# Optimization experiments

Measured on AMD Instinct MI355X. Metric: run time of the kernel, lower is better.

## Reference

```python
import jax, jax.numpy as jnp
import numpy as np

B, H, W, DM = 4, 64, 64, 96
DS, DC, K = 16, 3, 4
DI = DM            # expand = 1.0
DTR = 6            # ceil(96/16)


def setup_inputs() -> dict:
    key = jax.random.key(0)
    ks = jax.random.split(key, 12)
    s = 0.02
    # dt bias init exactly as MS2D.dt_init: dt ~ exp(U*(log(max)-log(min))+log(min)); inv softplus
    dt = jnp.exp(jax.random.uniform(ks[5], (K, DI)) * (np.log(0.1) - np.log(0.001)) + np.log(0.001))
    dt = jnp.clip(dt, 1e-4, None)
    inv_dt = dt + jnp.log(-jnp.expm1(-dt))
    A_logs = jnp.log(jnp.broadcast_to(jnp.arange(1, DS + 1, dtype=jnp.float32), (K, DI, DS)))
    return {
        "x": jax.random.normal(ks[0], (B, H, W, DM), jnp.float32),
        "in_proj_w": jax.random.normal(ks[1], (2 * DI, DM), jnp.float32) * s,
        "conv_w": jax.random.normal(ks[2], (DI, 1, DC, DC), jnp.float32) * s,
        "conv_b": jnp.zeros((DI,), jnp.float32),
        "x_proj_weight": jax.random.normal(ks[3], (K, DTR + 2 * DS, DI), jnp.float32) * s,
        "dt_projs_weight": jax.random.uniform(ks[4], (K, DI, DTR), minval=-1.0, maxval=1.0) * (DTR ** -0.5),
        "dt_projs_bias": inv_dt,
        "A_logs": A_logs,
        "Ds": jnp.ones((K, DI), jnp.float32),
        "out_norm_w": jnp.ones((DI,), jnp.float32),
        "out_norm_b": jnp.zeros((DI,), jnp.float32),
        "out_proj_w": jax.random.normal(ks[6], (DM, DI), jnp.float32) * s,
    }


def _ms2d(x, in_proj_w, conv_w, conv_b, x_proj_weight, dt_projs_weight,
          dt_projs_bias, A_logs, Ds, out_norm_w, out_norm_b, out_proj_w):
    Bb, Hh, Ww, _ = x.shape
    L = Hh * Ww
    # in_proj -> (x, z) gating split
    xz = x @ in_proj_w.T                      # (B,H,W,2*DI)
    xc, z = jnp.split(xz, 2, axis=-1)
    xc = jnp.transpose(xc, (0, 3, 1, 2))      # (B,DI,H,W)
    xc = jax.lax.conv_general_dilated(
        xc, conv_w, (1, 1), 'SAME', feature_group_count=xc.shape[1],
        dimension_numbers=('NCHW', 'OIHW', 'NCHW')) + conv_b[None, :, None, None]
    xc = jax.nn.silu(xc)
    d = xc.shape[1]
    # 4-directional scan sequences: hw, wh, and their reverses
    x_hw = xc.reshape(Bb, d, L)
    x_wh = jnp.transpose(xc, (0, 1, 3, 2)).reshape(Bb, d, L)
    x2 = jnp.stack([x_hw, x_wh], axis=1)          # (B,2,d,L)
    xs = jnp.concatenate([x2, jnp.flip(x2, axis=-1)], axis=1)  # (B,4,d,L)
    x_dbl = jnp.einsum('bkdl,kcd->bkcl', xs, x_proj_weight)
    dtr = dt_projs_weight.shape[2]
    n = A_logs.shape[2]
    dts, Bs, Cs = jnp.split(x_dbl, [dtr, dtr + n], axis=2)     # (B,4,r,L),(B,4,N,L),(B,4,N,L)
    dts = jnp.einsum('bkrl,kdr->bkdl', dts, dt_projs_weight)
    delta = jax.nn.softplus(dts + dt_projs_bias[None, :, :, None])  # (B,4,d,L)
    A = -jnp.exp(A_logs)                                        # (4,d,N)
    # time-major for scan
    u_t = jnp.moveaxis(xs, -1, 0)       # (L,B,4,d)
    dl_t = jnp.moveaxis(delta, -1, 0)
    B_t = jnp.moveaxis(Bs, -1, 0)       # (L,B,4,N)
    C_t = jnp.moveaxis(Cs, -1, 0)

    def step(h, inp):                   # h: (B,4,d,N)
        u, dl, b, c = inp
        dA = jnp.exp(dl[..., None] * A)
        h = h * dA + (dl * u)[..., None] * b[:, :, None, :]
        y = jnp.einsum('bkdn,bkn->bkd', h, c)
        return h, y

    h0 = jnp.zeros((Bb, 4, d, n), xs.dtype)
    _, ys = jax.lax.scan(step, h0, (u_t, dl_t, B_t, C_t))
    ys = jnp.moveaxis(ys, 0, -1)        # (B,4,d,L)
    ys = ys + Ds[None, :, :, None] * xs  # skip D*u
    inv_y = jnp.flip(ys[:, 2:4], axis=-1)

    def wh2hw(t):  # undo the (W,H) raster order
        return jnp.transpose(t.reshape(Bb, d, Ww, Hh), (0, 1, 3, 2)).reshape(Bb, d, L)

    y = ys[:, 0] + inv_y[:, 0] + wh2hw(ys[:, 1]) + wh2hw(inv_y[:, 1])
    y = jnp.transpose(y, (0, 2, 1)).reshape(Bb, Hh, Ww, d)
    mu = y.mean(-1, keepdims=True)
    var = y.var(-1, keepdims=True)
    y = (y - mu) / jnp.sqrt(var + 1e-5) * out_norm_w + out_norm_b
    y = y * jax.nn.silu(z)
    return y @ out_proj_w.T


def reference(x, in_proj_w, conv_w, conv_b, x_proj_weight, dt_projs_weight,
              dt_projs_bias, A_logs, Ds, out_norm_w, out_norm_b, out_proj_w):
    return _ms2d(x, in_proj_w, conv_w, conv_b, x_proj_weight, dt_projs_weight,
                 dt_projs_bias, A_logs, Ds, out_norm_w, out_norm_b, out_proj_w)
```

## Files before the change

### kernel.cpp

```cpp
#include <hip/hip_runtime.h>
#include <math.h>


#define LQ 4096
#define NCH 128
#define LCH 32

__device__ __forceinline__ float sigmoid_f(float x){ return 1.0f/(1.0f + __expf(-x)); }
__device__ __forceinline__ float silu_f(float x){ return x * sigmoid_f(x); }
__device__ __forceinline__ float softplus_f(float x){ return (x > 20.0f) ? x : __logf(1.0f + __expf(x)); }

__device__ __forceinline__ int pos_of(int k, int i){
  switch(k & 3){
    case 0: return i;
    case 1: return ((i & 63) << 6) | (i >> 6);
    case 2: return LQ - 1 - i;
    default: { int j = LQ - 1 - i; return ((j & 63) << 6) | (j >> 6); }
  }
}

__global__ __launch_bounds__(256) void k_inproj(const float* __restrict__ x,
                                                const float* __restrict__ wproj,
                                                float* __restrict__ xc,
                                                float* __restrict__ zb){
  __shared__ float a_s[64*97];
  __shared__ float w_s[192*97];
  const int t = threadIdx.x;
  const int row0 = blockIdx.x * 64;
  for (int e = t*4; e < 64*96; e += 1024){
    float4 v = *(const float4*)(x + row0*96 + e);
    int r = e/96, c = e%96;
    float* p = a_s + r*97 + c;
    p[0]=v.x; p[1]=v.y; p[2]=v.z; p[3]=v.w;
  }
  for (int e = t*4; e < 192*96; e += 1024){
    float4 v = *(const float4*)(wproj + e);
    int r = e/96, c = e%96;
    float* p = w_s + r*97 + c;
    p[0]=v.x; p[1]=v.y; p[2]=v.z; p[3]=v.w;
  }
  __syncthreads();
  const int tr = t >> 5, tc = t & 31;
  float acc[8][6];
  #pragma unroll
  for (int i=0;i<8;i++){
    #pragma unroll
    for (int j=0;j<6;j++) acc[i][j]=0.f;
  }
  for (int kk=0; kk<96; kk++){
    float a[8], b[6];
    #pragma unroll
    for (int i=0;i<8;i++) a[i] = a_s[(tr*8+i)*97+kk];
    #pragma unroll
    for (int j=0;j<6;j++) b[j] = w_s[(tc*6+j)*97+kk];
    #pragma unroll
    for (int i=0;i<8;i++){
      #pragma unroll
      for (int j=0;j<6;j++) acc[i][j] += a[i]*b[j];
    }
  }
  #pragma unroll
  for (int i=0;i<8;i++){
    int row = row0 + tr*8 + i;
    #pragma unroll
    for (int j=0;j<6;j++){
      int c = tc*6+j;
      float v = acc[i][j];
      if (c < 96) xc[row*96+c] = v;
      else        zb[row*96+(c-96)] = v;
    }
  }
}

__global__ __launch_bounds__(256) void k_conv(const float* __restrict__ xc,
                                              const float* __restrict__ cw,
                                              const float* __restrict__ cb,
                                              float* __restrict__ u){
  int e = blockIdx.x*256 + threadIdx.x;
  int d0 = (e % 24) * 4;
  int p = e / 24;
  int w = p & 63, h = (p >> 6) & 63, b = p >> 12;
  float cwv[4][9];
  #pragma unroll
  for (int q=0;q<4;q++){
    #pragma unroll
    for (int tp=0;tp<9;tp++) cwv[q][tp] = cw[(d0+q)*9+tp];
  }
  float4 acc = make_float4(cb[d0], cb[d0+1], cb[d0+2], cb[d0+3]);
  #pragma unroll
  for (int kh=0; kh<3; kh++){
    int hh = h + kh - 1;
    if (hh < 0 || hh > 63) continue;
    #pragma unroll
    for (int kw=0; kw<3; kw++){
      int ww = w + kw - 1;
      if (ww < 0 || ww > 63) continue;
      float4 v = *(const float4*)(xc + ((size_t)((b<<12) + (hh<<6) + ww))*96 + d0);
      int tp = kh*3+kw;
      acc.x += v.x*cwv[0][tp]; acc.y += v.y*cwv[1][tp];
      acc.z += v.z*cwv[2][tp]; acc.w += v.w*cwv[3][tp];
    }
  }
  float4 o = make_float4(silu_f(acc.x), silu_f(acc.y), silu_f(acc.z), silu_f(acc.w));
  *(float4*)(u + (size_t)p*96 + d0) = o;
}

__global__ __launch_bounds__(128) void k_proj(const float* __restrict__ u,
                                              const float* __restrict__ xpw,
                                              float* __restrict__ dts,
                                              float* __restrict__ Bsb,
                                              float* __restrict__ Csb){
  __shared__ float u_s[64*97];
  __shared__ float w_s[40*97];
  const int t = threadIdx.x;
  const int blk = blockIdx.x;
  const int pt = blk & 63, k = (blk >> 6) & 3, b = blk >> 8;
  const int p0 = pt * 64;
  for (int e = t*4; e < 64*96; e += 512){
    int pp = e/96, c = e%96;
    float4 v = *(const float4*)(u + ((size_t)((b<<12) + p0 + pp))*96 + c);
    float* p = u_s + pp*97 + c;
    p[0]=v.x; p[1]=v.y; p[2]=v.z; p[3]=v.w;
  }
  for (int e = t*4; e < 40*96; e += 512){
    int r = e/96, c = e%96;
    float4 v = (r < 38) ? *(const float4*)(xpw + (k*38+r)*96 + c)
                        : make_float4(0,0,0,0);
    float* p = w_s + r*97 + c;
    p[0]=v.x; p[1]=v.y; p[2]=v.z; p[3]=v.w;
  }
  __syncthreads();
  const int posg = t & 15, cg = t >> 4;
  float acc[4][5];
  #pragma unroll
  for (int i=0;i<4;i++){
    #pragma unroll
    for (int j=0;j<5;j++) acc[i][j]=0.f;
  }
  for (int dd=0; dd<96; dd++){
    float uu[4], wv[5];
    #pragma unroll
    for (int i=0;i<4;i++) uu[i] = u_s[(posg*4+i)*97+dd];
    #pragma unroll
    for (int j=0;j<5;j++) wv[j] = w_s[(cg*5+j)*97+dd];
    #pragma unroll
    for (int i=0;i<4;i++){
      #pragma unroll
      for (int j=0;j<5;j++) acc[i][j] += uu[i]*wv[j];
    }
  }
  #pragma unroll
  for (int i=0;i<4;i++){
    int p = p0 + posg*4 + i;
    int base = ((b*4+k)<<12) + p;
    #pragma unroll
    for (int j=0;j<5;j++){
      int c = cg*5 + j;
      float v = acc[i][j];
      if (c < 6)       dts[(size_t)base*6 + c] = v;
      else if (c < 22) Bsb[(size_t)base*16 + (c-6)] = v;
      else if (c < 38) Csb[(size_t)base*16 + (c-22)] = v;
    }
  }
}

__device__ __forceinline__ void pow8(float r, int nh, float* e){
  e[0]=r;
  e[1]=r*r;
  e[2]=e[1]*r;
  e[3]=e[1]*e[1];
  e[4]=e[3]*r;
  e[5]=e[3]*e[1];
  e[6]=e[3]*e[2];
  e[7]=e[3]*e[3];
  float m = nh ? e[7] : 1.0f;
  #pragma unroll
  for (int j=0;j<8;j++) e[j] *= m;
}

template<bool FAST>
__device__ __forceinline__ void scanA_loop(const float* up, const float2* dtp,
    const float4* Bp, long ustep, long dtstep, long bstep,
    const float* dtw, float bias, int nh, const float* An, float* h, float& sdelta){
  #pragma unroll 4
  for (int il=0; il<LCH; il++){
    const float uv = *up;
    float2 q0 = dtp[0], q1 = dtp[1], q2 = dtp[2];
    float accd = bias + dtw[0]*q0.x + dtw[1]*q0.y + dtw[2]*q1.x
                      + dtw[3]*q1.y + dtw[4]*q2.x + dtw[5]*q2.y;
    float delta = softplus_f(accd);
    sdelta += delta;
    float du = delta * uv;
    float4 b0 = Bp[0], b1 = Bp[1];
    float Bv[8] = {b0.x,b0.y,b0.z,b0.w, b1.x,b1.y,b1.z,b1.w};
    float e[8];
    if (FAST){ pow8(__expf(-delta), nh, e); }
    else {
      #pragma unroll
      for (int n=0;n<8;n++) e[n] = __expf(delta*An[n]);
    }
    #pragma unroll
    for (int n=0;n<8;n++) h[n] = h[n]*e[n] + du*Bv[n];
    up += ustep; dtp += dtstep; Bp += bstep;
  }
}

__global__ __launch_bounds__(384) void k_scanA(const float* __restrict__ u,
                                               const float* __restrict__ dts,
                                               const float* __restrict__ Bsb,
                                               const float* __restrict__ dtw_g,
                                               const float* __restrict__ dtb_g,
                                               const float* __restrict__ Alogs,
                                               float* __restrict__ S,
                                               float* __restrict__ sumd){
  const int t = threadIdx.x;
  const int c2 = t / 192;
  const int lane = t & 63;
  const int wv3 = (t % 192) >> 6;
  const int nh = (lane >> 5) & 1;
  const int d = wv3*32 + (lane & 31);
  const int blk = blockIdx.x;
  const int bk = blk >> 6;
  const int k = bk & 3, b = bk >> 2;
  const int chunk = ((blk & 63) << 1) | c2;
  float An[8];
  bool fast = true;
  #pragma unroll
  for (int j=0;j<8;j++){
    int n = nh*8 + j;
    An[j] = -__expf(Alogs[(k*96+d)*16+n]);
    fast = fast && (fabsf(An[j] + (float)(n+1)) < 1e-3f*(float)(n+1));
  }
  int wfast = __all(fast ? 1 : 0);
  float dtw[6];
  #pragma unroll
  for (int r=0;r<6;r++) dtw[r] = dtw_g[(k*96+d)*6+r];
  const float bias = dtb_g[k*96+d];
  const int i0 = chunk*LCH;
  const int pb = pos_of(k, i0);
  const int pstep = pos_of(k, i0+1) - pb;
  const float* up = u + ((size_t)((b<<12)+pb))*96 + d;
  const float2* dtp = (const float2*)(dts + ((size_t)((bk<<12)+pb))*6);
  const float4* Bp = (const float4*)(Bsb + ((size_t)((bk<<12)+pb))*16) + nh*2;
  const long ustep = (long)pstep*96;
  const long dtstep = (long)pstep*3;
  const long bstep = (long)pstep*4;
  float h[8];
  #pragma unroll
  for (int n=0;n<8;n++) h[n]=0.f;
  float sdelta = 0.f;
  if (wfast) scanA_loop<true >(up,dtp,Bp,ustep,dtstep,bstep,dtw,bias,nh,An,h,sdelta);
  else       scanA_loop<false>(up,dtp,Bp,ustep,dtstep,bstep,dtw,bias,nh,An,h,sdelta);
  const int sb = (bk*NCH + chunk)*96 + d;
  float4* Sp = (float4*)(S + (size_t)sb*16 + nh*8);
  Sp[0] = make_float4(h[0],h[1],h[2],h[3]);
  Sp[1] = make_float4(h[4],h[5],h[6],h[7]);
  if (nh == 0) sumd[sb] = sdelta;
}

__global__ __launch_bounds__(256) void k_scanB(const float* __restrict__ S,
                                               const float* __restrict__ sumd,
                                               const float* __restrict__ Alogs,
                                               float* __restrict__ hinit){
  const int t = blockIdx.x*256 + threadIdx.x;
  const int n = t & 15;
  const int d = (t >> 4) % 96;
  const int bk = t / 1536;
  const int k = bk & 3;
  const float An = -__expf(Alogs[(k*96+d)*16+n]);
  float h = 0.f;
  for (int c=0;c<NCH;c++){
    const int sb = (bk*NCH + c)*96 + d;
    hinit[(size_t)sb*16+n] = h;
    float P = __expf(An * sumd[sb]);
    h = h*P + S[(size_t)sb*16+n];
  }
}

template<bool FAST>
__device__ __forceinline__ void scanC_loop(const float* up, const float2* dtp,
    const float4* Bp, const float4* Cp, float* yp,
    long ustep, long dtstep, long bstep,
    const float* dtw, float bias, int nh, const float* An, float* h){
  #pragma unroll 4
  for (int il=0; il<LCH; il++){
    const float uv = *up;
    float2 q0 = dtp[0], q1 = dtp[1], q2 = dtp[2];
    float accd = bias + dtw[0]*q0.x + dtw[1]*q0.y + dtw[2]*q1.x
                      + dtw[3]*q1.y + dtw[4]*q2.x + dtw[5]*q2.y;
    float delta = softplus_f(accd);
    float du = delta * uv;
    float4 b0 = Bp[0], b1 = Bp[1];
    float4 c0 = Cp[0], c1 = Cp[1];
    float Bv[8] = {b0.x,b0.y,b0.z,b0.w, b1.x,b1.y,b1.z,b1.w};
    float Cv[8] = {c0.x,c0.y,c0.z,c0.w, c1.x,c1.y,c1.z,c1.w};
    float e[8];
    if (FAST){ pow8(__expf(-delta), nh, e); }
    else {
      #pragma unroll
      for (int n=0;n<8;n++) e[n] = __expf(delta*An[n]);
    }
    float y8 = 0.f;
    #pragma unroll
    for (int n=0;n<8;n++){
      h[n] = h[n]*e[n] + du*Bv[n];
      y8 += h[n]*Cv[n];
    }
    float y = y8 + __shfl_xor(y8, 32, 64);
    if (nh == 0) *yp = y;
    up += ustep; dtp += dtstep; Bp += bstep; Cp += bstep; yp += ustep;
  }
}

__global__ __launch_bounds__(384) void k_scanC(const float* __restrict__ u,
                                               const float* __restrict__ dts,
                                               const float* __restrict__ Bsb,
                                               const float* __restrict__ Csb,
                                               const float* __restrict__ dtw_g,
                                               const float* __restrict__ dtb_g,
                                               const float* __restrict__ Alogs,
                                               const float* __restrict__ hinit,
                                               float* __restrict__ ys){
  const int t = threadIdx.x;
  const int c2 = t / 192;
  const int lane = t & 63;
  const int wv3 = (t % 192) >> 6;
  const int nh = (lane >> 5) & 1;
  const int d = wv3*32 + (lane & 31);
  const int blk = blockIdx.x;
  const int bk = blk >> 6;
  const int k = bk & 3, b = bk >> 2;
  const int chunk = ((blk & 63) << 1) | c2;
  float An[8];
  bool fast = true;
  #pragma unroll
  for (int j=0;j<8;j++){
    int n = nh*8 + j;
    An[j] = -__expf(Alogs[(k*96+d)*16+n]);
    fast = fast && (fabsf(An[j] + (float)(n+1)) < 1e-3f*(float)(n+1));
  }
  int wfast = __all(fast ? 1 : 0);
  float dtw[6];
  #pragma unroll
  for (int r=0;r<6;r++) dtw[r] = dtw_g[(k*96+d)*6+r];
  const float bias = dtb_g[k*96+d];
  const int i0 = chunk*LCH;
  const int pb = pos_of(k, i0);
  const int pstep = pos_of(k, i0+1) - pb;
  const float* up = u + ((size_t)((b<<12)+pb))*96 + d;
  const float2* dtp = (const float2*)(dts + ((size_t)((bk<<12)+pb))*6);
  const float4* Bp = (const float4*)(Bsb + ((size_t)((bk<<12)+pb))*16) + nh*2;
  const float4* Cp = (const float4*)(Csb + ((size_t)((bk<<12)+pb))*16) + nh*2;
  float* yp = ys + ((size_t)((bk<<12)+pb))*96 + d;
  const long ustep = (long)pstep*96;
  const long dtstep = (long)pstep*3;
  const long bstep = (long)pstep*4;
  float h[8];
  const int sb = (bk*NCH + chunk)*96 + d;
  const float4* Hp = (const float4*)(hinit + (size_t)sb*16 + nh*8);
  {
    float4 h0=Hp[0], h1=Hp[1];
    h[0]=h0.x;h[1]=h0.y;h[2]=h0.z;h[3]=h0.w;
    h[4]=h1.x;h[5]=h1.y;h[6]=h1.z;h[7]=h1.w;
  }
  if (wfast) scanC_loop<true >(up,dtp,Bp,Cp,yp,ustep,dtstep,bstep,dtw,bias,nh,An,h);
  else       scanC_loop<false>(up,dtp,Bp,Cp,yp,ustep,dtstep,bstep,dtw,bias,nh,An,h);
}

__global__ __launch_bounds__(256) void k_out(const float* __restrict__ ys,
                                             const float* __restrict__ ubuf,
                                             const float* __restrict__ Dsg,
                                             const float* __restrict__ zbuf,
                                             const float* __restrict__ nw,
                                             const float* __restrict__ nb,
                                             const float* __restrict__ wout,
                                             float* __restrict__ out){
  __shared__ float w_s[96*97];
  __shared__ float g_s[64*97];
  __shared__ float redA[256];
  __shared__ float redB[256];
  const int t = threadIdx.x;
  const int b = blockIdx.x >> 6;
  const int pt = blockIdx.x & 63;
  const int p0 = pt * 64;
  for (int e=t*4; e<96*96; e+=1024){
    float4 v = *(const float4*)(wout+e);
    int r=e/96, c=e%96;
    float* p = w_s + r*97 + c;
    p[0]=v.x; p[1]=v.y; p[2]=v.z; p[3]=v.w;
  }
  const int pos2 = t >> 2, lane4 = t & 3, d0 = lane4*24;
  const int p = p0 + pos2;
  float yv[24];
  float s1=0.f, s2=0.f;
  #pragma unroll
  for (int i=0;i<24;i+=4){
    float4 a = make_float4(0,0,0,0);
    #pragma unroll
    for (int kk=0;kk<4;kk++){
      float4 v = *(const float4*)(ys + ((size_t)(((b*4+kk)<<12) + p))*96 + d0 + i);
      a.x+=v.x; a.y+=v.y; a.z+=v.z; a.w+=v.w;
    }
    float4 uv = *(const float4*)(ubuf + ((size_t)((b<<12)+p))*96 + d0 + i);
    #pragma unroll
    for (int q=0;q<4;q++){
      int dd = d0+i+q;
      float sD = Dsg[dd] + Dsg[96+dd] + Dsg[192+dd] + Dsg[288+dd];
      float uq = (q==0)?uv.x:(q==1)?uv.y:(q==2)?uv.z:uv.w;
      float* aq = (q==0)?&a.x:(q==1)?&a.y:(q==2)?&a.z:&a.w;
      *aq += sD * uq;
    }
    yv[i]=a.x; yv[i+1]=a.y; yv[i+2]=a.z; yv[i+3]=a.w;
    s1 += a.x+a.y+a.z+a.w;
    s2 += a.x*a.x + a.y*a.y + a.z*a.z + a.w*a.w;
  }
  redA[t]=s1; redB[t]=s2;
  __syncthreads();
  if (lane4 < 2){ redA[t]+=redA[t+2]; redB[t]+=redB[t+2]; }
  __syncthreads();
  if (lane4 < 1){ redA[t]+=redA[t+1]; redB[t]+=redB[t+1]; }
  __syncthreads();
  const float mu = redA[pos2*4] * (1.0f/96.0f);
  const float var = redB[pos2*4] * (1.0f/96.0f) - mu*mu;
  const float rstd = rsqrtf(var + 1e-5f);
  #pragma unroll
  for (int i=0;i<24;i+=4){
    float4 zv = *(const float4*)(zbuf + ((size_t)((b<<12)+p))*96 + d0 + i);
    float zz[4] = {zv.x,zv.y,zv.z,zv.w};
    #pragma unroll
    for (int q=0;q<4;q++){
      int d = d0+i+q;
      float yn = (yv[i+q]-mu)*rstd*nw[d] + nb[d];
      g_s[pos2*97 + d] = yn * silu_f(zz[q]);
    }
  }
  __syncthreads();
  const int posg = t >> 5, mg = t & 31;
  float acc[8][3];
  #pragma unroll
  for (int i=0;i<8;i++){
    #pragma unroll
    for (int j=0;j<3;j++) acc[i][j]=0.f;
  }
  for (int dd=0; dd<96; dd++){
    float g8[8], w3[3];
    #pragma unroll
    for (int i=0;i<8;i++) g8[i] = g_s[(posg*8+i)*97+dd];
    #pragma unroll
    for (int j=0;j<3;j++) w3[j] = w_s[(mg*3+j)*97+dd];
    #pragma unroll
    for (int i=0;i<8;i++){
      #pragma unroll
      for (int j=0;j<3;j++) acc[i][j] += g8[i]*w3[j];
    }
  }
  #pragma unroll
  for (int i=0;i<8;i++){
    int prow = p0 + posg*8 + i;
    #pragma unroll
    for (int j=0;j<3;j++){
      out[((size_t)((b<<12)+prow))*96 + mg*3 + j] = acc[i][j];
    }
  }
}

extern "C" void kernel_launch(void* const* d_in, const int* in_sizes, int n_in,
                              void* d_out, int out_size, void* d_ws, size_t ws_size,
                              hipStream_t stream) {
  (void)in_sizes; (void)n_in; (void)out_size; (void)ws_size;
  const float* x   = (const float*)d_in[0];
  const float* ipw = (const float*)d_in[1];
  const float* cw  = (const float*)d_in[2];
  const float* cb  = (const float*)d_in[3];
  const float* xpw = (const float*)d_in[4];
  const float* dtw = (const float*)d_in[5];
  const float* dtb = (const float*)d_in[6];
  const float* alg = (const float*)d_in[7];
  const float* dsg = (const float*)d_in[8];
  const float* nw  = (const float*)d_in[9];
  const float* nb  = (const float*)d_in[10];
  const float* wo  = (const float*)d_in[11];
  float* out = (float*)d_out;

  float* w = (float*)d_ws;
  size_t off = 0;
  float* z_b    = w + off; off += 1572864;
  float* u_b    = w + off; off += 1572864;
  float* dts_b  = w + off; off += 393216;
  float* Bs_b   = w + off; off += 1048576;
  float* Cs_b   = w + off; off += 1048576;
  float* hin_b  = w + off; off += 3145728;
  float* ys_b   = w + off; off += 6291456;
  float* xc_b   = ys_b;
  float* S_b    = ys_b + 1572864;
  float* sumd_b = ys_b + 1572864 + 3145728;

  k_inproj<<<256, 256, 0, stream>>>(x, ipw, xc_b, z_b);
  k_conv  <<<1536, 256, 0, stream>>>(xc_b, cw, cb, u_b);
  k_proj  <<<1024, 128, 0, stream>>>(u_b, xpw, dts_b, Bs_b, Cs_b);
  k_scanA <<<1024, 384, 0, stream>>>(u_b, dts_b, Bs_b, dtw, dtb, alg, S_b, sumd_b);
  k_scanB <<<96, 256, 0, stream>>>(S_b, sumd_b, alg, hin_b);
  k_scanC <<<1024, 384, 0, stream>>>(u_b, dts_b, Bs_b, Cs_b, dtw, dtb, alg, hin_b, ys_b);
  k_out   <<<256, 256, 0, stream>>>(ys_b, u_b, dsg, z_b, nw, nb, wo, out);
}
```

Measured before the change: 273.9 us.

## Stage scan inputs in LDS, precompute delta terms cooperatively, split GEMM blocks

Both scan kernels now load a 64-step tile of u, dt-projection and B/C rows into shared memory, using coalesced float4 loads along the scan order. All 384 threads then compute softplus(delta), delta*u and exp(-delta) for the tile before the recurrence runs. This removes the strided per-thread global loads and the duplicate delta computation that the two n-halves each did. The in-projection and output kernels are split into twice as many smaller blocks for more parallelism, and the output kernel's LayerNorm reduction switches from shared memory to wavefront shuffles. The cost is larger LDS use per scan block, which may lower occupancy, plus an extra barrier.

```diff
diff --git a/kernel.cpp b/kernel.cpp
--- a/kernel.cpp
+++ b/kernel.cpp
@@ -19,56 +19,67 @@
   }
 }
 
+__device__ __forceinline__ void pow8(float r, int nh, float* e){
+  e[0]=r;
+  e[1]=r*r;
+  e[2]=e[1]*r;
+  e[3]=e[1]*e[1];
+  e[4]=e[3]*r;
+  e[5]=e[3]*e[1];
+  e[6]=e[3]*e[2];
+  e[7]=e[3]*e[3];
+  float m = nh ? e[7] : 1.0f;
+  #pragma unroll
+  for (int j=0;j<8;j++) e[j] *= m;
+}
+
 __global__ __launch_bounds__(256) void k_inproj(const float* __restrict__ x,
                                                 const float* __restrict__ wproj,
                                                 float* __restrict__ xc,
                                                 float* __restrict__ zb){
   __shared__ float a_s[64*97];
-  __shared__ float w_s[192*97];
+  __shared__ float w_s[96*97];
   const int t = threadIdx.x;
-  const int row0 = blockIdx.x * 64;
+  const int row0 = (blockIdx.x >> 1) * 64;
+  const int ch = blockIdx.x & 1;
   for (int e = t*4; e < 64*96; e += 1024){
-    float4 v = *(const float4*)(x + row0*96 + e);
+    float4 v = *(const float4*)(x + (size_t)row0*96 + e);
     int r = e/96, c = e%96;
     float* p = a_s + r*97 + c;
     p[0]=v.x; p[1]=v.y; p[2]=v.z; p[3]=v.w;
   }
-  for (int e = t*4; e < 192*96; e += 1024){
-    float4 v = *(const float4*)(wproj + e);
+  for (int e = t*4; e < 96*96; e += 1024){
+    float4 v = *(const float4*)(wproj + (size_t)ch*96*96 + e);
     int r = e/96, c = e%96;
     float* p = w_s + r*97 + c;
     p[0]=v.x; p[1]=v.y; p[2]=v.z; p[3]=v.w;
   }
   __syncthreads();
   const int tr = t >> 5, tc = t & 31;
-  float acc[8][6];
+  float acc[8][3];
   #pragma unroll
   for (int i=0;i<8;i++){
     #pragma unroll
-    for (int j=0;j<6;j++) acc[i][j]=0.f;
+    for (int j=0;j<3;j++) acc[i][j]=0.f;
   }
   for (int kk=0; kk<96; kk++){
-    float a[8], b[6];
+    float a[8], b[3];
     #pragma unroll
     for (int i=0;i<8;i++) a[i] = a_s[(tr*8+i)*97+kk];
     #pragma unroll
-    for (int j=0;j<6;j++) b[j] = w_s[(tc*6+j)*97+kk];
+    for (int j=0;j<3;j++) b[j] = w_s[(tc*3+j)*97+kk];
     #pragma unroll
     for (int i=0;i<8;i++){
       #pragma unroll
-      for (int j=0;j<6;j++) acc[i][j] += a[i]*b[j];
-    }
-  }
+      for (int j=0;j<3;j++) acc[i][j] += a[i]*b[j];
+    }
+  }
+  float* dst = ch ? zb : xc;
   #pragma unroll
   for (int i=0;i<8;i++){
     int row = row0 + tr*8 + i;
     #pragma unroll
-    for (int j=0;j<6;j++){
-      int c = tc*6+j;
-      float v = acc[i][j];
-      if (c < 96) xc[row*96+c] = v;
-      else        zb[row*96+(c-96)] = v;
-    }
+    for (int j=0;j<3;j++) dst[(size_t)row*96 + tc*3 + j] = acc[i][j];
   }
 }
 
@@ -164,47 +175,6 @@
   }
 }
 
-__device__ __forceinline__ void pow8(float r, int nh, float* e){
-  e[0]=r;
-  e[1]=r*r;
-  e[2]=e[1]*r;
-  e[3]=e[1]*e[1];
-  e[4]=e[3]*r;
-  e[5]=e[3]*e[1];
-  e[6]=e[3]*e[2];
-  e[7]=e[3]*e[3];
-  float m = nh ? e[7] : 1.0f;
-  #pragma unroll
-  for (int j=0;j<8;j++) e[j] *= m;
-}
-
-template<bool FAST>
-__device__ __forceinline__ void scanA_loop(const float* up, const float2* dtp,
-    const float4* Bp, long ustep, long dtstep, long bstep,
-    const float* dtw, float bias, int nh, const float* An, float* h, float& sdelta){
-  #pragma unroll 4
-  for (int il=0; il<LCH; il++){
-    const float uv = *up;
-    float2 q0 = dtp[0], q1 = dtp[1], q2 = dtp[2];
-    float accd = bias + dtw[0]*q0.x + dtw[1]*q0.y + dtw[2]*q1.x
-                      + dtw[3]*q1.y + dtw[4]*q2.x + dtw[5]*q2.y;
-    float delta = softplus_f(accd);
-    sdelta += delta;
-    float du = delta * uv;
-    float4 b0 = Bp[0], b1 = Bp[1];
-    float Bv[8] = {b0.x,b0.y,b0.z,b0.w, b1.x,b1.y,b1.z,b1.w};
-    float e[8];
-    if (FAST){ pow8(__expf(-delta), nh, e); }
-    else {
-      #pragma unroll
-      for (int n=0;n<8;n++) e[n] = __expf(delta*An[n]);
-    }
-    #pragma unroll
-    for (int n=0;n<8;n++) h[n] = h[n]*e[n] + du*Bv[n];
-    up += ustep; dtp += dtstep; Bp += bstep;
-  }
-}
-
 __global__ __launch_bounds__(384) void k_scanA(const float* __restrict__ u,
                                                const float* __restrict__ dts,
                                                const float* __restrict__ Bsb,
@@ -213,16 +183,63 @@
                                                const float* __restrict__ Alogs,
                                                float* __restrict__ S,
                                                float* __restrict__ sumd){
+  __shared__ float du_s[64*96];
+  __shared__ float r_s[64*96];
+  __shared__ float dt_s[64*8];
+  __shared__ float B_s[64*16];
+  __shared__ float sd_part[4*96];
   const int t = threadIdx.x;
+  const int blk = blockIdx.x;
+  const int bk = blk >> 6;
+  const int k = bk & 3, b = bk >> 2;
+  const int chunk0 = (blk & 63) << 1;
+  for (int e = t*4; e < 64*96; e += 1536){
+    int row = e/96, c = e%96;
+    int p = pos_of(k, (chunk0 + (row>>5))*LCH + (row&31));
+    float4 v = *(const float4*)(u + ((size_t)((b<<12)+p))*96 + c);
+    float* dst = du_s + row*96 + c;
+    dst[0]=v.x; dst[1]=v.y; dst[2]=v.z; dst[3]=v.w;
+  }
+  {
+    int row = t/6, j = t - row*6;
+    int p = pos_of(k, (chunk0 + (row>>5))*LCH + (row&31));
+    dt_s[row*8+j] = dts[((size_t)((bk<<12)+p))*6 + j];
+  }
+  if (t < 256){
+    int row = t>>2, q = t&3;
+    int p = pos_of(k, (chunk0 + (row>>5))*LCH + (row&31));
+    float4 v = *(const float4*)(Bsb + ((size_t)((bk<<12)+p))*16 + q*4);
+    *(float4*)(B_s + row*16 + q*4) = v;
+  }
+  __syncthreads();
+  {
+    const int d = t % 96, g = t / 96;
+    const int c2 = g >> 1, il0 = (g & 1) * 16;
+    float dtwv[6];
+    #pragma unroll
+    for (int r=0;r<6;r++) dtwv[r] = dtw_g[(k*96+d)*6+r];
+    const float bias = dtb_g[k*96+d];
+    float sd = 0.f;
+    #pragma unroll 4
+    for (int il = il0; il < il0+16; il++){
+      int row = c2*32 + il;
+      const float* dr = dt_s + row*8;
+      float accd = bias + dr[0]*dtwv[0] + dr[1]*dtwv[1] + dr[2]*dtwv[2]
+                        + dr[3]*dtwv[3] + dr[4]*dtwv[4] + dr[5]*dtwv[5];
+      float delta = softplus_f(accd);
+      sd += delta;
+      int idx = row*96 + d;
+      du_s[idx] = delta * du_s[idx];
+      r_s[idx] = __expf(-delta);
+    }
+    sd_part[g*96 + d] = sd;
+  }
+  __syncthreads();
   const int c2 = t / 192;
   const int lane = t & 63;
   const int wv3 = (t % 192) >> 6;
   const int nh = (lane >> 5) & 1;
   const int d = wv3*32 + (lane & 31);
-  const int blk = blockIdx.x;
-  const int bk = blk >> 6;
-  const int k = bk & 3, b = bk >> 2;
-  const int chunk = ((blk & 63) << 1) | c2;
   float An[8];
   bool fast = true;
   #pragma unroll
@@ -232,30 +249,46 @@
     fast = fast && (fabsf(An[j] + (float)(n+1)) < 1e-3f*(float)(n+1));
   }
   int wfast = __all(fast ? 1 : 0);
-  float dtw[6];
-  #pragma unroll
-  for (int r=0;r<6;r++) dtw[r] = dtw_g[(k*96+d)*6+r];
-  const float bias = dtb_g[k*96+d];
-  const int i0 = chunk*LCH;
-  const int pb = pos_of(k, i0);
-  const int pstep = pos_of(k, i0+1) - pb;
-  const float* up = u + ((size_t)((b<<12)+pb))*96 + d;
-  const float2* dtp = (const float2*)(dts + ((size_t)((bk<<12)+pb))*6);
-  const float4* Bp = (const float4*)(Bsb + ((size_t)((bk<<12)+pb))*16) + nh*2;
-  const long ustep = (long)pstep*96;
-  const long dtstep = (long)pstep*3;
-  const long bstep = (long)pstep*4;
   float h[8];
   #pragma unroll
   for (int n=0;n<8;n++) h[n]=0.f;
-  float sdelta = 0.f;
-  if (wfast) scanA_loop<true >(up,dtp,Bp,ustep,dtstep,bstep,dtw,bias,nh,An,h,sdelta);
-  else       scanA_loop<false>(up,dtp,Bp,ustep,dtstep,bstep,dtw,bias,nh,An,h,sdelta);
-  const int sb = (bk*NCH + chunk)*96 + d;
+  const float* dup = du_s + c2*32*96 + d;
+  const float* rp  = r_s  + c2*32*96 + d;
+  const float* Bb  = B_s + c2*32*16 + nh*8;
+  if (wfast){
+    #pragma unroll 4
+    for (int il=0; il<LCH; il++){
+      float r = rp[il*96];
+      float du = dup[il*96];
+      const float4* Bp = (const float4*)(Bb + il*16);
+      float4 b0 = Bp[0], b1 = Bp[1];
+      float Bv[8] = {b0.x,b0.y,b0.z,b0.w, b1.x,b1.y,b1.z,b1.w};
+      float e[8];
+      pow8(r, nh, e);
+      #pragma unroll
+      for (int n=0;n<8;n++) h[n] = h[n]*e[n] + du*Bv[n];
+    }
+  } else {
+    #pragma unroll 2
+    for (int il=0; il<LCH; il++){
+      float r = rp[il*96];
+      float delta = -__logf(r);
+      float du = dup[il*96];
+      const float4* Bp = (const float4*)(Bb + il*16);
+      float4 b0 = Bp[0], b1 = Bp[1];
+      float Bv[8] = {b0.x,b0.y,b0.z,b0.w, b1.x,b1.y,b1.z,b1.w};
+      float e[8];
+      #pragma unroll
+      for (int n=0;n<8;n++) e[n] = __expf(delta*An[n]);
+      #pragma unroll
+      for (int n=0;n<8;n++) h[n] = h[n]*e[n] + du*Bv[n];
+    }
+  }
+  const int sb = (bk*NCH + chunk0 + c2)*96 + d;
   float4* Sp = (float4*)(S + (size_t)sb*16 + nh*8);
   Sp[0] = make_float4(h[0],h[1],h[2],h[3]);
   Sp[1] = make_float4(h[4],h[5],h[6],h[7]);
-  if (nh == 0) sumd[sb] = sdelta;
+  if (nh == 0) sumd[sb] = sd_part[(c2*2)*96 + d] + sd_part[(c2*2+1)*96 + d];
 }
 
 __global__ __launch_bounds__(256) void k_scanB(const float* __restrict__ S,
@@ -277,41 +310,6 @@
   }
 }
 
-template<bool FAST>
-__device__ __forceinline__ void scanC_loop(const float* up, const float2* dtp,
-    const float4* Bp, const float4* Cp, float* yp,
-    long ustep, long dtstep, long bstep,
-    const float* dtw, float bias, int nh, const float* An, float* h){
-  #pragma unroll 4
-  for (int il=0; il<LCH; il++){
-    const float uv = *up;
-    float2 q0 = dtp[0], q1 = dtp[1], q2 = dtp[2];
-    float accd = bias + dtw[0]*q0.x + dtw[1]*q0.y + dtw[2]*q1.x
-                      + dtw[3]*q1.y + dtw[4]*q2.x + dtw[5]*q2.y;
-    float delta = softplus_f(accd);
-    float du = delta * uv;
-    float4 b0 = Bp[0], b1 = Bp[1];
-    float4 c0 = Cp[0], c1 = Cp[1];
-    float Bv[8] = {b0.x,b0.y,b0.z,b0.w, b1.x,b1.y,b1.z,b1.w};
-    float Cv[8] = {c0.x,c0.y,c0.z,c0.w, c1.x,c1.y,c1.z,c1.w};
-    float e[8];
-    if (FAST){ pow8(__expf(-delta), nh, e); }
-    else {
-      #pragma unroll
-      for (int n=0;n<8;n++) e[n] = __expf(delta*An[n]);
-    }
-    float y8 = 0.f;
-    #pragma unroll
-    for (int n=0;n<8;n++){
-      h[n] = h[n]*e[n] + du*Bv[n];
-      y8 += h[n]*Cv[n];
-    }
-    float y = y8 + __shfl_xor(y8, 32, 64);
-    if (nh == 0) *yp = y;
-    up += ustep; dtp += dtstep; Bp += bstep; Cp += bstep; yp += ustep;
-  }
-}
-
 __global__ __launch_bounds__(384) void k_scanC(const float* __restrict__ u,
                                                const float* __restrict__ dts,
                                                const float* __restrict__ Bsb,
@@ -321,16 +319,62 @@
                                                const float* __restrict__ Alogs,
                                                const float* __restrict__ hinit,
                                                float* __restrict__ ys){
+  __shared__ float du_s[64*96];
+  __shared__ float r_s[64*96];
+  __shared__ float dt_s[64*8];
+  __shared__ float B_s[64*16];
+  __shared__ float C_s[64*16];
   const int t = threadIdx.x;
+  const int blk = blockIdx.x;
+  const int bk = blk >> 6;
+  const int k = bk & 3, b = bk >> 2;
+  const int chunk0 = (blk & 63) << 1;
+  for (int e = t*4; e < 64*96; e += 1536){
+    int row = e/96, c = e%96;
+    int p = pos_of(k, (chunk0 + (row>>5))*LCH + (row&31));
+    float4 v = *(const float4*)(u + ((size_t)((b<<12)+p))*96 + c);
+    float* dst = du_s + row*96 + c;
+    dst[0]=v.x; dst[1]=v.y; dst[2]=v.z; dst[3]=v.w;
+  }
+  {
+    int row = t/6, j = t - row*6;
+    int p = pos_of(k, (chunk0 + (row>>5))*LCH + (row&31));
+    dt_s[row*8+j] = dts[((size_t)((bk<<12)+p))*6 + j];
+  }
+  if (t < 256){
+    int row = t>>2, q = t&3;
+    int p = pos_of(k, (chunk0 + (row>>5))*LCH + (row&31));
+    float4 v = *(const float4*)(Bsb + ((size_t)((bk<<12)+p))*16 + q*4);
+    *(float4*)(B_s + row*16 + q*4) = v;
+    float4 w = *(const float4*)(Csb + ((size_t)((bk<<12)+p))*16 + q*4);
+    *(float4*)(C_s + row*16 + q*4) = w;
+  }
+  __syncthreads();
+  {
+    const int d = t % 96, g = t / 96;
+    const int c2 = g >> 1, il0 = (g & 1) * 16;
+    float dtwv[6];
+    #pragma unroll
+    for (int r=0;r<6;r++) dtwv[r] = dtw_g[(k*96+d)*6+r];
+    const float bias = dtb_g[k*96+d];
+    #pragma unroll 4
+    for (int il = il0; il < il0+16; il++){
+      int row = c2*32 + il;
+      const float* dr = dt_s + row*8;
+      float accd = bias + dr[0]*dtwv[0] + dr[1]*dtwv[1] + dr[2]*dtwv[2]
+                        + dr[3]*dtwv[3] + dr[4]*dtwv[4] + dr[5]*dtwv[5];
+      float delta = softplus_f(accd);
+      int idx = row*96 + d;
+      du_s[idx] = delta * du_s[idx];
+      r_s[idx] = __expf(-delta);
+    }
+  }
+  __syncthreads();
   const int c2 = t / 192;
   const int lane = t & 63;
   const int wv3 = (t % 192) >> 6;
   const int nh = (lane >> 5) & 1;
   const int d = wv3*32 + (lane & 31);
-  const int blk = blockIdx.x;
-  const int bk = blk >> 6;
-  const int k = bk & 3, b = bk >> 2;
-  const int chunk = ((blk & 63) << 1) | c2;
   float An[8];
   bool fast = true;
   #pragma unroll
@@ -340,21 +384,12 @@
     fast = fast && (fabsf(An[j] + (float)(n+1)) < 1e-3f*(float)(n+1));
   }
   int wfast = __all(fast ? 1 : 0);
-  float dtw[6];
-  #pragma unroll
-  for (int r=0;r<6;r++) dtw[r] = dtw_g[(k*96+d)*6+r];
-  const float bias = dtb_g[k*96+d];
+  const int chunk = chunk0 + c2;
   const int i0 = chunk*LCH;
   const int pb = pos_of(k, i0);
   const int pstep = pos_of(k, i0+1) - pb;
-  const float* up = u + ((size_t)((b<<12)+pb))*96 + d;
-  const float2* dtp = (const float2*)(dts + ((size_t)((bk<<12)+pb))*6);
-  const float4* Bp = (const float4*)(Bsb + ((size_t)((bk<<12)+pb))*16) + nh*2;
-  const float4* Cp = (const float4*)(Csb + ((size_t)((bk<<12)+pb))*16) + nh*2;
   float* yp = ys + ((size_t)((bk<<12)+pb))*96 + d;
-  const long ustep = (long)pstep*96;
-  const long dtstep = (long)pstep*3;
-  const long bstep = (long)pstep*4;
+  const long ystep = (long)pstep*96;
   float h[8];
   const int sb = (bk*NCH + chunk)*96 + d;
   const float4* Hp = (const float4*)(hinit + (size_t)sb*16 + nh*8);
@@ -363,8 +398,57 @@
     h[0]=h0.x;h[1]=h0.y;h[2]=h0.z;h[3]=h0.w;
     h[4]=h1.x;h[5]=h1.y;h[6]=h1.z;h[7]=h1.w;
   }
-  if (wfast) scanC_loop<true >(up,dtp,Bp,Cp,yp,ustep,dtstep,bstep,dtw,bias,nh,An,h);
-  else       scanC_loop<false>(up,dtp,Bp,Cp,yp,ustep,dtstep,bstep,dtw,bias,nh,An,h);
+  const float* dup = du_s + c2*32*96 + d;
+  const float* rp  = r_s  + c2*32*96 + d;
+  const float* Bb  = B_s + c2*32*16 + nh*8;
+  const float* Cb  = C_s + c2*32*16 + nh*8;
+  if (wfast){
+    #pragma unroll 4
+    for (int il=0; il<LCH; il++){
+      float r = rp[il*96];
+      float du = dup[il*96];
+      const float4* Bp = (const float4*)(Bb + il*16);
+      const float4* Cp = (const float4*)(Cb + il*16);
+      float4 b0 = Bp[0], b1 = Bp[1];
+      float4 c0 = Cp[0], c1 = Cp[1];
+      float Bv[8] = {b0.x,b0.y,b0.z,b0.w, b1.x,b1.y,b1.z,b1.w};
+      float Cv[8] = {c0.x,c0.y,c0.z,c0.w, c1.x,c1.y,c1.z,c1.w};
+      float e[8];
+      pow8(r, nh, e);
+      float y8 = 0.f;
+      #pragma unroll
+      for (int n=0;n<8;n++){
+        h[n] = h[n]*e[n] + du*Bv[n];
+        y8 += h[n]*Cv[n];
+      }
+      float y = y8 + __shfl_xor(y8, 32, 64);
+      if (nh == 0) yp[il*ystep] = y;
+    }
+  } else {
+    #pragma unroll 2
+    for (int il=0; il<LCH; il++){
+      float r = rp[il*96];
+      float delta = -__logf(r);
+      float du = dup[il*96];
+      const float4* Bp = (const float4*)(Bb + il*16);
+      const float4* Cp = (const float4*)(Cb + il*16);
+      float4 b0 = Bp[0], b1 = Bp[1];
+      float4 c0 = Cp[0], c1 = Cp[1];
+      float Bv[8] = {b0.x,b0.y,b0.z,b0.w, b1.x,b1.y,b1.z,b1.w};
+      float Cv[8] = {c0.x,c0.y,c0.z,c0.w, c1.x,c1.y,c1.z,c1.w};
+      float e[8];
+      #pragma unroll
+      for (int n=0;n<8;n++) e[n] = __expf(delta*An[n]);
+      float y8 = 0.f;
+      #pragma unroll
+      for (int n=0;n<8;n++){
+        h[n] = h[n]*e[n] + du*Bv[n];
+        y8 += h[n]*Cv[n];
+      }
+      float y = y8 + __shfl_xor(y8, 32, 64);
+      if (nh == 0) yp[il*ystep] = y;
+    }
+  }
 }
 
 __global__ __launch_bounds__(256) void k_out(const float* __restrict__ ys,
@@ -376,25 +460,23 @@
                                              const float* __restrict__ wout,
                                              float* __restrict__ out){
   __shared__ float w_s[96*97];
-  __shared__ float g_s[64*97];
-  __shared__ float redA[256];
-  __shared__ float redB[256];
+  __shared__ float g_s[32*97];
   const int t = threadIdx.x;
-  const int b = blockIdx.x >> 6;
-  const int pt = blockIdx.x & 63;
-  const int p0 = pt * 64;
+  const int b = blockIdx.x >> 7;
+  const int pt = blockIdx.x & 127;
+  const int p0 = pt * 32;
   for (int e=t*4; e<96*96; e+=1024){
     float4 v = *(const float4*)(wout+e);
     int r=e/96, c=e%96;
     float* p = w_s + r*97 + c;
     p[0]=v.x; p[1]=v.y; p[2]=v.z; p[3]=v.w;
   }
-  const int pos2 = t >> 2, lane4 = t & 3, d0 = lane4*24;
-  const int p = p0 + pos2;
-  float yv[24];
+  const int pos = t >> 3, lane8 = t & 7, d0 = lane8*12;
+  const int p = p0 + pos;
+  float yv[12];
   float s1=0.f, s2=0.f;
   #pragma unroll
-  for (int i=0;i<24;i+=4){
+  for (int i=0;i<12;i+=4){
     float4 a = make_float4(0,0,0,0);
     #pragma unroll
     for (int kk=0;kk<4;kk++){
@@ -414,49 +496,48 @@
     s1 += a.x+a.y+a.z+a.w;
     s2 += a.x*a.x + a.y*a.y + a.z*a.z + a.w*a.w;
   }
-  redA[t]=s1; redB[t]=s2;
-  __syncthreads();
-  if (lane4 < 2){ redA[t]+=redA[t+2]; redB[t]+=redB[t+2]; }
-  __syncthreads();
-  if (lane4 < 1){ redA[t]+=redA[t+1]; redB[t]+=redB[t+1]; }
-  __syncthreads();
-  const float mu = redA[pos2*4] * (1.0f/96.0f);
-  const float var = redB[pos2*4] * (1.0f/96.0f) - mu*mu;
+  #pragma unroll
+  for (int m=1; m<8; m<<=1){
+    s1 += __shfl_xor(s1, m, 64);
+    s2 += __shfl_xor(s2, m, 64);
+  }
+  const float mu = s1 * (1.0f/96.0f);
+  const float var = s2 * (1.0f/96.0f) - mu*mu;
   const float rstd = rsqrtf(var + 1e-5f);
   #pragma unroll
-  for (int i=0;i<24;i+=4){
+  for (int i=0;i<12;i+=4){
     float4 zv = *(const float4*)(zbuf + ((size_t)((b<<12)+p))*96 + d0 + i);
     float zz[4] = {zv.x,zv.y,zv.z,zv.w};
     #pragma unroll
     for (int q=0;q<4;q++){
       int d = d0+i+q;
       float yn = (yv[i+q]-mu)*rstd*nw[d] + nb[d];
-      g_s[pos2*97 + d] = yn * silu_f(zz[q]);
+      g_s[pos*97 + d] = yn * silu_f(zz[q]);
     }
   }
   __syncthreads();
   const int posg = t >> 5, mg = t & 31;
-  float acc[8][3];
-  #pragma unroll
-  for (int i=0;i<8;i++){
+  float acc[4][3];
+  #pragma unroll
+  for (int i=0;i<4;i++){
     #pragma unroll
     for (int j=0;j<3;j++) acc[i][j]=0.f;
   }
   for (int dd=0; dd<96; dd++){
-    float g8[8], w3[3];
-    #pragma unroll
-    for (int i=0;i<8;i++) g8[i] = g_s[(posg*8+i)*97+dd];
+    float g4[4], w3[3];
+    #pragma unroll
+    for (int i=0;i<4;i++) g4[i] = g_s[(posg*4+i)*97+dd];
     #pragma unroll
     for (int j=0;j<3;j++) w3[j] = w_s[(mg*3+j)*97+dd];
     #pragma unroll
-    for (int i=0;i<8;i++){
-      #pragma unroll
-      for (int j=0;j<3;j++) acc[i][j] += g8[i]*w3[j];
-    }
-  }
-  #pragma unroll
-  for (int i=0;i<8;i++){
-    int prow = p0 + posg*8 + i;
+    for (int i=0;i<4;i++){
+      #pragma unroll
+      for (int j=0;j<3;j++) acc[i][j] += g4[i]*w3[j];
+    }
+  }
+  #pragma unroll
+  for (int i=0;i<4;i++){
+    int prow = p0 + posg*4 + i;
     #pragma unroll
     for (int j=0;j<3;j++){
       out[((size_t)((b<<12)+prow))*96 + mg*3 + j] = acc[i][j];
@@ -495,11 +576,11 @@
   float* S_b    = ys_b + 1572864;
   float* sumd_b = ys_b + 1572864 + 3145728;
 
-  k_inproj<<<256, 256, 0, stream>>>(x, ipw, xc_b, z_b);
+  k_inproj<<<512, 256, 0, stream>>>(x, ipw, xc_b, z_b);
   k_conv  <<<1536, 256, 0, stream>>>(xc_b, cw, cb, u_b);
   k_proj  <<<1024, 128, 0, stream>>>(u_b, xpw, dts_b, Bs_b, Cs_b);
   k_scanA <<<1024, 384, 0, stream>>>(u_b, dts_b, Bs_b, dtw, dtb, alg, S_b, sumd_b);
   k_scanB <<<96, 256, 0, stream>>>(S_b, sumd_b, alg, hin_b);
   k_scanC <<<1024, 384, 0, stream>>>(u_b, dts_b, Bs_b, Cs_b, dtw, dtb, alg, hin_b, ys_b);
-  k_out   <<<256, 256, 0, stream>>>(ys_b, u_b, dsg, z_b, nw, nb, wo, out);
-}
+  k_out   <<<512, 256, 0, stream>>>(ys_b, u_b, dsg, z_b, nw, nb, wo, out);
+}
```

After: 241.1 us. 12.0% less time.
